# Optimization experiments

Measured on AMD Instinct MI355X. Metric: run time of the kernel, lower is better.

Reference implementation:

```python
import jax, jax.numpy as jnp
import numpy as np

N = 100000      # nodes
E = 1600000     # nonzeros in sparse H (avg degree 16)
IN_DIM = 128
HID = 128
OUT = 128


def setup_inputs() -> dict:
    key = jax.random.key(0)
    k = jax.random.split(key, 8)
    X = jax.random.normal(k[0], (N, IN_DIM), dtype=jnp.float32)
    H_rows = jax.random.randint(k[1], (E,), 0, N, dtype=jnp.int32)
    H_cols = jax.random.randint(k[2], (E,), 0, N, dtype=jnp.int32)
    H_vals = jax.random.uniform(k[3], (E,), dtype=jnp.float32)
    # Linear params (PyTorch: y = x @ W.T + b); store as [in, out] for x @ W
    s1 = 1.0 / np.sqrt(IN_DIM)
    s2 = 1.0 / np.sqrt(HID)
    W1 = jax.random.uniform(k[4], (IN_DIM, HID), jnp.float32, -s1, s1)
    b1 = jax.random.uniform(k[5], (HID,), jnp.float32, -s1, s1)
    W2 = jax.random.uniform(k[6], (HID, OUT), jnp.float32, -s2, s2)
    b2 = jax.random.uniform(k[7], (OUT,), jnp.float32, -s2, s2)
    return {"X": X, "H_rows": H_rows, "H_cols": H_cols, "H_vals": H_vals,
            "W1": W1, "b1": b1, "W2": W2, "b2": b2}


def _spmm(rows, cols, vals, X):
    # sparse [N,N] @ dense [N,d] via edge gather + segment-sum
    msgs = vals[:, None] * X[cols]            # [E, d]
    return jax.ops.segment_sum(msgs, rows, num_segments=N)


def reference(X, H_rows, H_cols, H_vals, W1, b1, W2, b2):
    # num_layers == 2 branch; dropout is identity (eval mode)
    h = _spmm(H_rows, H_cols, H_vals, X @ W1 + b1)   # H @ W1(X)
    h = jax.nn.relu(h)
    out = _spmm(H_rows, H_cols, H_vals, h @ W2 + b2) # H @ W2(h)
    return out
```

## Files before the change

### kernel.cpp

```cpp
#include <hip/hip_runtime.h>

#define NNODES 100000
#define DIM 128
#define BROWS 256
#define NB ((NNODES + BROWS - 1) / BROWS)
#define BCAP 5120
#define CHUNK 4096

typedef _Float16 half8 __attribute__((ext_vector_type(8)));
typedef float f32x4 __attribute__((ext_vector_type(4)));
typedef unsigned int u32x4 __attribute__((ext_vector_type(4)));
typedef unsigned long long u64;

__device__ __forceinline__ unsigned int pack_bf16x2(float lo, float hi) {
    unsigned int ul = __float_as_uint(lo);
    unsigned int uh = __float_as_uint(hi);
    ul = (ul + 0x7fffu + ((ul >> 16) & 1u)) >> 16;
    uh = (uh + 0x7fffu + ((uh >> 16) & 1u)) & 0xffff0000u;
    return uh | ul;
}

__device__ __forceinline__ void unpack_bf16x8_v(u32x4 v, float* f) {
    f[0] = __uint_as_float(v.x << 16); f[1] = __uint_as_float(v.x & 0xffff0000u);
    f[2] = __uint_as_float(v.y << 16); f[3] = __uint_as_float(v.y & 0xffff0000u);
    f[4] = __uint_as_float(v.z << 16); f[5] = __uint_as_float(v.z & 0xffff0000u);
    f[6] = __uint_as_float(v.w << 16); f[7] = __uint_as_float(v.w & 0xffff0000u);
}

template <bool IN_BF16>
__device__ __forceinline__ void gemm_body(int blk, const void* __restrict__ Ain,
                                          const _Float16* __restrict__ Wt,
                                          const float* __restrict__ bias,
                                          unsigned short* __restrict__ Yb, int n) {
    const int t = threadIdx.x;
    const int l = t & 63;
    const int lr = l & 15;
    const int lg = l >> 4;
    const int r0 = blk * 128 + (t >> 6) * 32;

    half8 xf[2][4];
#pragma unroll
    for (int rt = 0; rt < 2; ++rt) {
        const int row = r0 + rt * 16 + lr;
        const bool ok = row < n;
        if (IN_BF16) {
            const u32x4* __restrict__ A16 = (const u32x4*)Ain;
#pragma unroll
            for (int ks = 0; ks < 4; ++ks) {
                u32x4 v = {0u, 0u, 0u, 0u};
                if (ok) v = A16[(size_t)row * 16 + ks * 4 + lg];
                float f[8];
                unpack_bf16x8_v(v, f);
                half8 h;
#pragma unroll
                for (int j = 0; j < 8; ++j) h[j] = (_Float16)f[j];
                xf[rt][ks] = h;
            }
        } else {
            const f32x4* __restrict__ A4 = (const f32x4*)Ain;
#pragma unroll
            for (int ks = 0; ks < 4; ++ks) {
                f32x4 v0 = {0.f, 0.f, 0.f, 0.f};
                f32x4 v1 = v0;
                if (ok) {
                    v0 = A4[(size_t)row * 32 + ks * 8 + lg * 2];
                    v1 = A4[(size_t)row * 32 + ks * 8 + lg * 2 + 1];
                }
                half8 h;
                h[0] = (_Float16)v0.x; h[1] = (_Float16)v0.y;
                h[2] = (_Float16)v0.z; h[3] = (_Float16)v0.w;
                h[4] = (_Float16)v1.x; h[5] = (_Float16)v1.y;
                h[6] = (_Float16)v1.z; h[7] = (_Float16)v1.w;
                xf[rt][ks] = h;
            }
        }
    }

    const f32x4 zero4 = {0.f, 0.f, 0.f, 0.f};
    f32x4 acc[2][8];
#pragma unroll
    for (int rt = 0; rt < 2; ++rt)
#pragma unroll
        for (int ct = 0; ct < 8; ++ct) acc[rt][ct] = zero4;

    const half8* __restrict__ Wf = (const half8*)Wt;
#pragma unroll
    for (int ct = 0; ct < 8; ++ct) {
        half8 wf[4];
#pragma unroll
        for (int ks = 0; ks < 4; ++ks)
            wf[ks] = Wf[(ct * 16 + lr) * 16 + ks * 4 + lg];
#pragma unroll
        for (int ks = 0; ks < 4; ++ks) {
            acc[0][ct] = __builtin_amdgcn_mfma_f32_16x16x32_f16(wf[ks], xf[0][ks], acc[0][ct], 0, 0, 0);
            acc[1][ct] = __builtin_amdgcn_mfma_f32_16x16x32_f16(wf[ks], xf[1][ks], acc[1][ct], 0, 0, 0);
        }
    }

#pragma unroll
    for (int ct = 0; ct < 8; ++ct) {
        const int c0 = ct * 16 + lg * 4;
        const float4 bv = *(const float4*)&bias[c0];
#pragma unroll
        for (int rt = 0; rt < 2; ++rt) {
            const int row = r0 + rt * 16 + lr;
            if (row < n) {
                f32x4 a = acc[rt][ct];
                const uint2 pv = make_uint2(pack_bf16x2(a[0] + bv.x, a[1] + bv.y),
                                            pack_bf16x2(a[2] + bv.z, a[3] + bv.w));
                *(uint2*)&Yb[(size_t)row * DIM + c0] = pv;
            }
        }
    }
}

__global__ __launch_bounds__(256) void pass1_bin(const int* __restrict__ rows,
                                                 const int* __restrict__ cols,
                                                 const float* __restrict__ vals,
                                                 int* __restrict__ bcnt,
                                                 int2* __restrict__ tmp, int nnz,
                                                 int p1_blocks,
                                                 const float* __restrict__ W1s,
                                                 const float* __restrict__ W2s,
                                                 _Float16* __restrict__ Wt1,
                                                 _Float16* __restrict__ Wt2) {
    __shared__ int hist[NB];
    __shared__ int base[NB];
    __shared__ int cur[NB];
    const int t = threadIdx.x;

    if (blockIdx.x >= (unsigned)p1_blocks) {
        const int b = blockIdx.x - p1_blocks;
        const float* __restrict__ W = (b & 4) ? W2s : W1s;
        _Float16* __restrict__ Wt = (b & 4) ? Wt2 : Wt1;
        const int base2 = (b & 3) * 4096;
        for (int i = t; i < 4096; i += 256) {
            const int e = base2 + i;
            const int k = e >> 7, c = e & 127;
            Wt[c * 128 + k] = (_Float16)W[e];
        }
        return;
    }

    const int e0 = blockIdx.x * CHUNK;
    const int e1 = min(e0 + CHUNK, nnz);

    for (int i = t; i < NB; i += 256) { hist[i] = 0; cur[i] = 0; }
    __syncthreads();

    for (int i = e0 + t; i < e1; i += 256)
        atomicAdd(&hist[rows[i] >> 8], 1);
    __syncthreads();

    for (int i = t; i < NB; i += 256)
        base[i] = (hist[i] > 0) ? atomicAdd(&bcnt[i], hist[i]) : 0;
    __syncthreads();

    for (int i = e0 + t; i < e1; i += 256) {
        const int r = rows[i];
        const int b = r >> 8;
        const int pos = base[b] + atomicAdd(&cur[b], 1);
        if (pos < BCAP)
            tmp[(size_t)b * BCAP + pos] =
                make_int2(((r & 255) << 24) | cols[i], __float_as_int(vals[i]));
    }
}

__global__ __launch_bounds__(256) void pass2_gemm1(const int2* __restrict__ tmp,
                                                   const int* __restrict__ bcnt,
                                                   int2* __restrict__ epack,
                                                   int* __restrict__ row_ptr,
                                                   int* __restrict__ counts,
                                                   const float* __restrict__ X,
                                                   const _Float16* __restrict__ Wt1,
                                                   const float* __restrict__ b1,
                                                   unsigned short* __restrict__ Yb, int n) {
    __shared__ int cnt[256];
    __shared__ int s[256];
    __shared__ int cur[256];

    if (blockIdx.x >= NB) {
        gemm_body<false>(blockIdx.x - NB, X, Wt1, b1, Yb, n);
        return;
    }

    const int b = blockIdx.x;
    const int t = threadIdx.x;
    const int row0 = b * BROWS;
    const int nrows = min(BROWS, n - row0);
    const int m = min(bcnt[b], BCAP);
    const int2* __restrict__ src = tmp + (size_t)b * BCAP;

    int partial = 0;
    for (int i = t; i < b; i += 256) partial += bcnt[i];
    s[t] = partial;
    __syncthreads();
    for (int off = 128; off >= 1; off >>= 1) {
        if (t < off) s[t] += s[t + off];
        __syncthreads();
    }
    const int base = s[0];
    __syncthreads();

    cnt[t] = 0;
    __syncthreads();
    for (int i = t; i < m; i += 256)
        atomicAdd(&cnt[((unsigned)src[i].x) >> 24], 1);
    __syncthreads();

    const int v = cnt[t];
    s[t] = v;
    __syncthreads();
    for (int off = 1; off < 256; off <<= 1) {
        int x = (t >= off) ? s[t - off] : 0;
        __syncthreads();
        s[t] += x;
        __syncthreads();
    }
    const int excl = s[t] - v;
    if (t < nrows) {
        row_ptr[row0 + t] = base + excl;
        counts[row0 + t] = v;
    }
    cur[t] = base + excl;
    __syncthreads();

    for (int i = t; i < m; i += 256) {
        const int2 e = src[i];
        const int rl = ((unsigned)e.x) >> 24;
        const int pos = atomicAdd(&cur[rl], 1);
        epack[pos] = make_int2(e.x & 0xFFFFFF, e.y);
    }
}

__global__ __launch_bounds__(256) void spmm1_gemm2(const int* __restrict__ row_ptr,
                                                   const int* __restrict__ counts,
                                                   const int2* __restrict__ epack,
                                                   const unsigned short* __restrict__ Xb,
                                                   const _Float16* __restrict__ Wt2,
                                                   const float* __restrict__ bias,
                                                   unsigned short* __restrict__ Yb2, int n) {
    __shared__ _Float16 hl[4][16][136];
    const int t = threadIdx.x;
    const int w = t >> 6;
    const int l = t & 63;
    const int rloc = l >> 2;
    const int q = l & 3;
    const int rbase = blockIdx.x * 64 + w * 16;
    const int r = rbase + rloc;

    float acc[32];
#pragma unroll
    for (int k = 0; k < 32; ++k) acc[k] = 0.f;

    if (r < n) {
        const int start = row_ptr[r];
        const int cnt = counts[r];
        const u32x4* __restrict__ X16 = (const u32x4*)Xb;
        const u64* __restrict__ ep = (const u64*)(epack + start);
        int j = 0;
        for (; j + 2 <= cnt; j += 2) {
            const u64 e0 = ep[j], e1 = ep[j + 1];
            const size_t b0 = (size_t)(unsigned)(e0 & 0xffffffffu) * 16 + q;
            const size_t b1 = (size_t)(unsigned)(e1 & 0xffffffffu) * 16 + q;
            u32x4 x0[4], x1[4];
#pragma unroll
            for (int p2 = 0; p2 < 4; ++p2) { x0[p2] = X16[b0 + p2 * 4]; x1[p2] = X16[b1 + p2 * 4]; }
            const float v0 = __uint_as_float((unsigned)(e0 >> 32));
            const float v1 = __uint_as_float((unsigned)(e1 >> 32));
#pragma unroll
            for (int p2 = 0; p2 < 4; ++p2) {
                float f0[8], f1[8];
                unpack_bf16x8_v(x0[p2], f0); unpack_bf16x8_v(x1[p2], f1);
#pragma unroll
                for (int k = 0; k < 8; ++k)
                    acc[p2 * 8 + k] += v0 * f0[k] + v1 * f1[k];
            }
        }
        if (j < cnt) {
            const u64 e = ep[j];
            const size_t b0 = (size_t)(unsigned)(e & 0xffffffffu) * 16 + q;
            const float v = __uint_as_float((unsigned)(e >> 32));
#pragma unroll
            for (int p2 = 0; p2 < 4; ++p2) {
                const u32x4 x = X16[b0 + p2 * 4];
                float f[8];
                unpack_bf16x8_v(x, f);
#pragma unroll
                for (int k = 0; k < 8; ++k) acc[p2 * 8 + k] = fmaf(v, f[k], acc[p2 * 8 + k]);
            }
        }
    }

#pragma unroll
    for (int p2 = 0; p2 < 4; ++p2) {
        half8 h;
#pragma unroll
        for (int k = 0; k < 8; ++k) h[k] = (_Float16)fmaxf(acc[p2 * 8 + k], 0.f);
        *(half8*)&hl[w][rloc][p2 * 32 + q * 8] = h;
    }
    asm volatile("s_waitcnt lgkmcnt(0)" ::: "memory");
    __builtin_amdgcn_sched_barrier(0);

    const int lr = l & 15;
    const int lg = l >> 4;
    half8 hf[4];
#pragma unroll
    for (int ks = 0; ks < 4; ++ks)
        hf[ks] = *(const half8*)&hl[w][lr][ks * 32 + lg * 8];

    const half8* __restrict__ Wf = (const half8*)Wt2;
    const int orow = rbase + lr;
#pragma unroll
    for (int ct = 0; ct < 8; ++ct) {
        f32x4 a2 = {0.f, 0.f, 0.f, 0.f};
#pragma unroll
        for (int ks = 0; ks < 4; ++ks) {
            const half8 wf = Wf[(ct * 16 + lr) * 16 + ks * 4 + lg];
            a2 = __builtin_amdgcn_mfma_f32_16x16x32_f16(wf, hf[ks], a2, 0, 0, 0);
        }
        const int c0 = ct * 16 + lg * 4;
        const float4 bv = *(const float4*)&bias[c0];
        if (orow < n) {
            const uint2 pv = make_uint2(pack_bf16x2(a2[0] + bv.x, a2[1] + bv.y),
                                        pack_bf16x2(a2[2] + bv.z, a2[3] + bv.w));
            *(uint2*)&Yb2[(size_t)orow * DIM + c0] = pv;
        }
    }
}

__global__ __launch_bounds__(256) void spmm_csr(const int* __restrict__ row_ptr,
                                                const int* __restrict__ counts,
                                                const int2* __restrict__ epack,
                                                const unsigned short* __restrict__ Xb,
                                                float* __restrict__ out, int n) {
    const int gid = blockIdx.x * blockDim.x + threadIdx.x;
    const int r = gid >> 4;
    const int lane = gid & 15;
    if (r >= n) return;
    const int start = row_ptr[r];
    const int cnt = counts[r];
    const u32x4* __restrict__ X16 = (const u32x4*)Xb;
    const u64* __restrict__ ep = (const u64*)(epack + start);

    float acc[8];
#pragma unroll
    for (int k = 0; k < 8; ++k) acc[k] = 0.f;

    int j = 0;
    for (; j + 8 <= cnt; j += 8) {
        u64 e[8];
#pragma unroll
        for (int q = 0; q < 8; ++q) e[q] = ep[j + q];
        u32x4 x[8];
#pragma unroll
        for (int q = 0; q < 8; ++q)
            x[q] = X16[(size_t)(unsigned)(e[q] & 0xffffffffu) * 16 + lane];
#pragma unroll
        for (int q = 0; q < 8; ++q) {
            const float v = __uint_as_float((unsigned)(e[q] >> 32));
            float f[8];
            unpack_bf16x8_v(x[q], f);
#pragma unroll
            for (int k = 0; k < 8; ++k) acc[k] = fmaf(v, f[k], acc[k]);
        }
    }
    for (; j + 2 <= cnt; j += 2) {
        const u64 e0 = ep[j], e1 = ep[j + 1];
        const u32x4 x0 = X16[(size_t)(unsigned)(e0 & 0xffffffffu) * 16 + lane];
        const u32x4 x1 = X16[(size_t)(unsigned)(e1 & 0xffffffffu) * 16 + lane];
        const float v0 = __uint_as_float((unsigned)(e0 >> 32));
        const float v1 = __uint_as_float((unsigned)(e1 >> 32));
        float f0[8], f1[8];
        unpack_bf16x8_v(x0, f0); unpack_bf16x8_v(x1, f1);
#pragma unroll
        for (int k = 0; k < 8; ++k)
            acc[k] += v0 * f0[k] + v1 * f1[k];
    }
    if (j < cnt) {
        const u64 e = ep[j];
        const u32x4 x = X16[(size_t)(unsigned)(e & 0xffffffffu) * 16 + lane];
        const float v = __uint_as_float((unsigned)(e >> 32));
        float f[8];
        unpack_bf16x8_v(x, f);
#pragma unroll
        for (int k = 0; k < 8; ++k) acc[k] = fmaf(v, f[k], acc[k]);
    }

    f32x4 a0 = {acc[0], acc[1], acc[2], acc[3]};
    f32x4 a1 = {acc[4], acc[5], acc[6], acc[7]};
    __builtin_nontemporal_store(a0, (f32x4*)&out[(size_t)r * DIM + lane * 8]);
    __builtin_nontemporal_store(a1, (f32x4*)&out[(size_t)r * DIM + lane * 8 + 4]);
}

extern "C" void kernel_launch(void* const* d_in, const int* in_sizes, int n_in,
                              void* d_out, int out_size, void* d_ws, size_t ws_size,
                              hipStream_t stream) {
    const float* X      = (const float*)d_in[0];
    const int*   H_rows = (const int*)d_in[1];
    const int*   H_cols = (const int*)d_in[2];
    const float* H_vals = (const float*)d_in[3];
    const float* W1     = (const float*)d_in[4];
    const float* b1     = (const float*)d_in[5];
    const float* W2     = (const float*)d_in[6];
    const float* b2     = (const float*)d_in[7];
    float* out = (float*)d_out;

    const int E = in_sizes[1];
    const int N = NNODES;
    const size_t bmat_bytes = (size_t)N * DIM * 2;

    const int gemm_blocks = (N + 127) / 128;
    const int p1_blocks = (E + CHUNK - 1) / CHUNK;
    const int fused_blocks = (N + 63) / 64;
    const int spmm_blocks = (N * 16 + 255) / 256;

    char* p = (char*)d_ws;
    unsigned short* Yb  = (unsigned short*)p; p += bmat_bytes;
    unsigned short* Yb2 = (unsigned short*)p; p += bmat_bytes;
    _Float16* Wt1      = (_Float16*)p;        p += 128 * 128 * 2;
    _Float16* Wt2      = (_Float16*)p;        p += 128 * 128 * 2;
    int2* epack        = (int2*)p;            p += (size_t)E * 8;
    int2* tmp          = (int2*)p;            p += (size_t)NB * BCAP * 8;
    int*  bcnt         = (int*)p;             p += (size_t)NB * 4;
    int*  row_ptr      = (int*)p;             p += (size_t)N * 4;
    int*  counts       = (int*)p;             p += (size_t)N * 4;

    hipMemsetAsync(bcnt, 0, (size_t)NB * 4, stream);
    pass1_bin<<<p1_blocks + 8, 256, 0, stream>>>(H_rows, H_cols, H_vals, bcnt, tmp, E,
                                                 p1_blocks, W1, W2, Wt1, Wt2);

    pass2_gemm1<<<NB + gemm_blocks, 256, 0, stream>>>(tmp, bcnt, epack, row_ptr, counts,
                                                      X, Wt1, b1, Yb, N);

    spmm1_gemm2<<<fused_blocks, 256, 0, stream>>>(row_ptr, counts, epack, Yb, Wt2, b2, Yb2, N);

    spmm_csr<<<spmm_blocks, 256, 0, stream>>>(row_ptr, counts, epack, Yb2, out, N);
}
```

Before: 347.8 us.

## Distribute fused SpMM edges across block threads with shared-memory atomic accumulation

The fused first SpMM plus second GEMM kernel now handles 16 rows per block. Instead of one row per thread group, each block walks the flat edge range of its 16 rows, and 16 slots of 16 lanes scatter each edge's contribution into a shared fp32 tile with LDS atomics. To make this possible, the local row index is packed into bits 20-23 of each edge's column word, and column indices are masked to 20 bits everywhere. The goal is to balance uneven row degrees and give each load wider, coalesced gathers. The cost is LDS atomic traffic, a tile zeroing pass, and four times as many blocks, each with a smaller GEMM share.

```diff
diff --git a/kernel.cpp b/kernel.cpp
--- a/kernel.cpp
+++ b/kernel.cpp
@@ -6,6 +6,7 @@
 #define NB ((NNODES + BROWS - 1) / BROWS)
 #define BCAP 5120
 #define CHUNK 4096
+#define HS 132
 
 typedef _Float16 half8 __attribute__((ext_vector_type(8)));
 typedef float f32x4 __attribute__((ext_vector_type(4)));
@@ -229,90 +230,86 @@
         const int2 e = src[i];
         const int rl = ((unsigned)e.x) >> 24;
         const int pos = atomicAdd(&cur[rl], 1);
-        epack[pos] = make_int2(e.x & 0xFFFFFF, e.y);
+        epack[pos] = make_int2(((rl & 15) << 20) | (e.x & 0xFFFFF), e.y);
     }
 }
 
 __global__ __launch_bounds__(256) void spmm1_gemm2(const int* __restrict__ row_ptr,
-                                                   const int* __restrict__ counts,
                                                    const int2* __restrict__ epack,
                                                    const unsigned short* __restrict__ Xb,
                                                    const _Float16* __restrict__ Wt2,
                                                    const float* __restrict__ bias,
-                                                   unsigned short* __restrict__ Yb2, int n) {
-    __shared__ _Float16 hl[4][16][136];
+                                                   unsigned short* __restrict__ Yb2,
+                                                   int n, int nnz) {
+    __shared__ float h[16][HS];
     const int t = threadIdx.x;
-    const int w = t >> 6;
+    const int slot = t >> 4;
+    const int lane = t & 15;
+    const int r0 = blockIdx.x * 16;
+
+    for (int i = t; i < 16 * HS; i += 256) ((float*)h)[i] = 0.f;
+    __syncthreads();
+
+    const int ps = row_ptr[r0];
+    const int pe = (r0 + 16 < n) ? row_ptr[r0 + 16] : nnz;
+    const u32x4* __restrict__ X16 = (const u32x4*)Xb;
+    const u64* __restrict__ ep = (const u64*)epack;
+
+    int i = ps + slot;
+    for (; i + 16 < pe; i += 32) {
+        const u64 e0 = ep[i], e1 = ep[i + 16];
+        const u32x4 x0 = X16[(size_t)(unsigned)(e0 & 0xFFFFFu) * 16 + lane];
+        const u32x4 x1 = X16[(size_t)(unsigned)(e1 & 0xFFFFFu) * 16 + lane];
+        const int rl0 = (int)((e0 >> 20) & 15), rl1 = (int)((e1 >> 20) & 15);
+        const float v0 = __uint_as_float((unsigned)(e0 >> 32));
+        const float v1 = __uint_as_float((unsigned)(e1 >> 32));
+        float f0[8], f1[8];
+        unpack_bf16x8_v(x0, f0); unpack_bf16x8_v(x1, f1);
+        float* h0 = &h[rl0][lane * 8];
+        float* h1 = &h[rl1][lane * 8];
+#pragma unroll
+        for (int j = 0; j < 8; ++j) {
+            const int jj = (j + lane) & 7;
+            atomicAdd(&h0[jj], v0 * f0[jj]);
+            atomicAdd(&h1[jj], v1 * f1[jj]);
+        }
+    }
+    if (i < pe) {
+        const u64 e = ep[i];
+        const u32x4 x = X16[(size_t)(unsigned)(e & 0xFFFFFu) * 16 + lane];
+        const int rl = (int)((e >> 20) & 15);
+        const float v = __uint_as_float((unsigned)(e >> 32));
+        float f[8];
+        unpack_bf16x8_v(x, f);
+        float* h0 = &h[rl][lane * 8];
+#pragma unroll
+        for (int j = 0; j < 8; ++j) {
+            const int jj = (j + lane) & 7;
+            atomicAdd(&h0[jj], v * f[jj]);
+        }
+    }
+    __syncthreads();
+
     const int l = t & 63;
-    const int rloc = l >> 2;
-    const int q = l & 3;
-    const int rbase = blockIdx.x * 64 + w * 16;
-    const int r = rbase + rloc;
-
-    float acc[32];
-#pragma unroll
-    for (int k = 0; k < 32; ++k) acc[k] = 0.f;
-
-    if (r < n) {
-        const int start = row_ptr[r];
-        const int cnt = counts[r];
-        const u32x4* __restrict__ X16 = (const u32x4*)Xb;
-        const u64* __restrict__ ep = (const u64*)(epack + start);
-        int j = 0;
-        for (; j + 2 <= cnt; j += 2) {
-            const u64 e0 = ep[j], e1 = ep[j + 1];
-            const size_t b0 = (size_t)(unsigned)(e0 & 0xffffffffu) * 16 + q;
-            const size_t b1 = (size_t)(unsigned)(e1 & 0xffffffffu) * 16 + q;
-            u32x4 x0[4], x1[4];
-#pragma unroll
-            for (int p2 = 0; p2 < 4; ++p2) { x0[p2] = X16[b0 + p2 * 4]; x1[p2] = X16[b1 + p2 * 4]; }
-            const float v0 = __uint_as_float((unsigned)(e0 >> 32));
-            const float v1 = __uint_as_float((unsigned)(e1 >> 32));
-#pragma unroll
-            for (int p2 = 0; p2 < 4; ++p2) {
-                float f0[8], f1[8];
-                unpack_bf16x8_v(x0[p2], f0); unpack_bf16x8_v(x1[p2], f1);
-#pragma unroll
-                for (int k = 0; k < 8; ++k)
-                    acc[p2 * 8 + k] += v0 * f0[k] + v1 * f1[k];
-            }
-        }
-        if (j < cnt) {
-            const u64 e = ep[j];
-            const size_t b0 = (size_t)(unsigned)(e & 0xffffffffu) * 16 + q;
-            const float v = __uint_as_float((unsigned)(e >> 32));
-#pragma unroll
-            for (int p2 = 0; p2 < 4; ++p2) {
-                const u32x4 x = X16[b0 + p2 * 4];
-                float f[8];
-                unpack_bf16x8_v(x, f);
-#pragma unroll
-                for (int k = 0; k < 8; ++k) acc[p2 * 8 + k] = fmaf(v, f[k], acc[p2 * 8 + k]);
-            }
-        }
-    }
-
-#pragma unroll
-    for (int p2 = 0; p2 < 4; ++p2) {
-        half8 h;
-#pragma unroll
-        for (int k = 0; k < 8; ++k) h[k] = (_Float16)fmaxf(acc[p2 * 8 + k], 0.f);
-        *(half8*)&hl[w][rloc][p2 * 32 + q * 8] = h;
-    }
-    asm volatile("s_waitcnt lgkmcnt(0)" ::: "memory");
-    __builtin_amdgcn_sched_barrier(0);
-
     const int lr = l & 15;
     const int lg = l >> 4;
+    const int w = t >> 6;
+
     half8 hf[4];
 #pragma unroll
-    for (int ks = 0; ks < 4; ++ks)
-        hf[ks] = *(const half8*)&hl[w][lr][ks * 32 + lg * 8];
+    for (int ks = 0; ks < 4; ++ks) {
+        const float* src = &h[lr][ks * 32 + lg * 8];
+        half8 hv;
+#pragma unroll
+        for (int k = 0; k < 8; ++k) hv[k] = (_Float16)fmaxf(src[k], 0.f);
+        hf[ks] = hv;
+    }
 
     const half8* __restrict__ Wf = (const half8*)Wt2;
-    const int orow = rbase + lr;
-#pragma unroll
-    for (int ct = 0; ct < 8; ++ct) {
+    const int orow = r0 + lr;
+#pragma unroll
+    for (int ct2 = 0; ct2 < 2; ++ct2) {
+        const int ct = w * 2 + ct2;
         f32x4 a2 = {0.f, 0.f, 0.f, 0.f};
 #pragma unroll
         for (int ks = 0; ks < 4; ++ks) {
@@ -355,7 +352,7 @@
         u32x4 x[8];
 #pragma unroll
         for (int q = 0; q < 8; ++q)
-            x[q] = X16[(size_t)(unsigned)(e[q] & 0xffffffffu) * 16 + lane];
+            x[q] = X16[(size_t)(unsigned)(e[q] & 0xFFFFFu) * 16 + lane];
 #pragma unroll
         for (int q = 0; q < 8; ++q) {
             const float v = __uint_as_float((unsigned)(e[q] >> 32));
@@ -367,8 +364,8 @@
     }
     for (; j + 2 <= cnt; j += 2) {
         const u64 e0 = ep[j], e1 = ep[j + 1];
-        const u32x4 x0 = X16[(size_t)(unsigned)(e0 & 0xffffffffu) * 16 + lane];
-        const u32x4 x1 = X16[(size_t)(unsigned)(e1 & 0xffffffffu) * 16 + lane];
+        const u32x4 x0 = X16[(size_t)(unsigned)(e0 & 0xFFFFFu) * 16 + lane];
+        const u32x4 x1 = X16[(size_t)(unsigned)(e1 & 0xFFFFFu) * 16 + lane];
         const float v0 = __uint_as_float((unsigned)(e0 >> 32));
         const float v1 = __uint_as_float((unsigned)(e1 >> 32));
         float f0[8], f1[8];
@@ -379,7 +376,7 @@
     }
     if (j < cnt) {
         const u64 e = ep[j];
-        const u32x4 x = X16[(size_t)(unsigned)(e & 0xffffffffu) * 16 + lane];
+        const u32x4 x = X16[(size_t)(unsigned)(e & 0xFFFFFu) * 16 + lane];
         const float v = __uint_as_float((unsigned)(e >> 32));
         float f[8];
         unpack_bf16x8_v(x, f);
@@ -412,7 +409,7 @@
 
     const int gemm_blocks = (N + 127) / 128;
     const int p1_blocks = (E + CHUNK - 1) / CHUNK;
-    const int fused_blocks = (N + 63) / 64;
+    const int fused_blocks = (N + 15) / 16;
     const int spmm_blocks = (N * 16 + 255) / 256;
 
     char* p = (char*)d_ws;
@@ -433,7 +430,7 @@
     pass2_gemm1<<<NB + gemm_blocks, 256, 0, stream>>>(tmp, bcnt, epack, row_ptr, counts,
                                                       X, Wt1, b1, Yb, N);
 
-    spmm1_gemm2<<<fused_blocks, 256, 0, stream>>>(row_ptr, counts, epack, Yb, Wt2, b2, Yb2, N);
+    spmm1_gemm2<<<fused_blocks, 256, 0, stream>>>(row_ptr, epack, Yb, Wt2, b2, Yb2, N, E);
 
     spmm_csr<<<spmm_blocks, 256, 0, stream>>>(row_ptr, counts, epack, Yb2, out, N);
 }
```

Measured after the change: 1.308 ms. 276% more time.
